# Optimization experiments

Hardware: AMD Instinct MI355X
Metric: run time of the kernel (lower is better)

Reference implementation:

```python
import jax, jax.numpy as jnp
import numpy as np
import math

HEADS = 4
LN_EPS = 1e-5


def _layer_norm(x, gamma, beta):
    # LayerNorm over last dim (N=4096), matching nn.LayerNorm(4096)
    mu = jnp.mean(x, axis=-1, keepdims=True)
    var = jnp.mean((x - mu) ** 2, axis=-1, keepdims=True)
    return (x - mu) * jax.lax.rsqrt(var + LN_EPS) * gamma + beta


def setup_inputs() -> dict:
    key = jax.random.key(0)
    ks = jax.random.split(key, 10)
    L, IMG, N = 1024, 1024, 4096
    s_img = 1.0 / math.sqrt(IMG)
    s_L = 1.0 / math.sqrt(L)
    return {
        "point_features": jax.random.normal(ks[0], (1, L, N), jnp.float32),
        "img_features": jax.random.normal(ks[1], (1, IMG, N), jnp.float32),
        # 4 per-head 1x1 convs IMG_chl -> L_chl
        "W_img": jax.random.normal(ks[2], (HEADS, L, IMG), jnp.float32) * s_img,
        "b_img": jax.random.normal(ks[3], (HEADS, L), jnp.float32) * s_img,
        # conv_L: L_chl -> L_chl
        "W_L": jax.random.normal(ks[4], (L, L), jnp.float32) * s_L,
        "b_L": jax.random.normal(ks[5], (L,), jnp.float32) * s_L,
        # LayerNorm(4096)
        "ln_g": jnp.ones((N,), jnp.float32),
        "ln_b": jnp.zeros((N,), jnp.float32),
        # conv_fusion: L_chl -> L_chl
        "W_f": jax.random.normal(ks[6], (L, L), jnp.float32) * s_L,
        "b_f": jax.random.normal(ks[7], (L,), jnp.float32) * s_L,
    }


def reference(point_features, img_features, W_img, b_img, W_L, b_L, ln_g, ln_b, W_f, b_f):
    # L_query = conv_L(point_features): [1, L, N]
    L_query = jnp.einsum('oi,bin->bon', W_L, point_features) + b_L[None, :, None]
    dk = L_query.shape[1]
    N = L_query.shape[2]

    # All 4 head keys at once: [H, 1, L, N]
    keys = jnp.einsum('hoi,bin->hbon', W_img, img_features) + b_img[:, None, :, None]

    # score_i = sum_c(key_i * query) / sqrt(dk)  -> cat over heads: [H, N] (B=1)
    score = jnp.sum(keys * L_query[None], axis=2).reshape(HEADS, N) / jnp.sqrt(jnp.float32(dk))

    # softmax across heads (dim=0), weightmap = [1, H, N]
    weight = jax.nn.softmax(score, axis=0)
    weightmap = weight[None]

    # z = sum_h weight[h] * key_h : [1, L, N]
    z = jnp.einsum('hn,hbcn->bcn', weight, keys)

    fused = _layer_norm(z + L_query, ln_g, ln_b)
    fusion_features = jnp.einsum('oi,bin->bon', W_f, fused) + b_f[None, :, None]
    return (fusion_features, weightmap)
```

## Files before the change

kernel.cpp:

```cpp
#include <hip/hip_runtime.h>
#include <hip/hip_bf16.h>
#include <stdint.h>

using u16 = unsigned short;

typedef __attribute__((ext_vector_type(8))) short bf16x8;
typedef __attribute__((ext_vector_type(4))) float f32x4;

typedef const __attribute__((address_space(1))) unsigned int* gas_t;
typedef __attribute__((address_space(3))) unsigned int* las_t;

__device__ inline void g2l16(const u16* g, u16* l) {
  __builtin_amdgcn_global_load_lds((gas_t)g, (las_t)l, 16, 0, 0);
}

__device__ inline u16 f2b(float x) {
  union { float f; uint32_t u; } v; v.f = x;
  uint32_t r = (v.u + 0x7FFFu + ((v.u >> 16) & 1u)) >> 16;
  return (u16)r;
}
__device__ inline float b2f(u16 b) {
  union { uint32_t u; float f; } v; v.u = ((uint32_t)b) << 16;
  return v.f;
}
__device__ inline float b2f_lo(uint32_t p) {
  union { uint32_t u; float f; } v; v.u = p << 16; return v.f;
}
__device__ inline float b2f_hi(uint32_t p) {
  union { uint32_t u; float f; } v; v.u = p & 0xFFFF0000u; return v.f;
}

__device__ inline void store_out(float* p, float v) { *p = v; }
__device__ inline void store_out(u16* p, float v) { *p = f2b(v); }

template<typename OutT>
__device__ inline void gemm_tile_128(const u16* __restrict__ A,
                                     const u16* __restrict__ Bt,
                                     const float* __restrict__ bias,
                                     OutT* __restrict__ C,
                                     int m0, int n0, int N, int K,
                                     u16* As, u16* Bs)
{
  const int tid  = threadIdx.x;
  const int wave = tid >> 6;
  const int lane = tid & 63;
  const int wm = wave >> 1, wn = wave & 1;
  const int lr = lane & 15;
  const int lq = lane >> 4;
  const int x7 = lr & 7;

  const int srow = tid >> 3;
  const int sgc  = (tid & 7) ^ (srow & 7);
  const u16* gA = A  + (size_t)(m0 + srow) * K + sgc * 8;
  const u16* gB = Bt + (size_t)(n0 + srow) * K + sgc * 8;
  u16* dstA = As + wave * 512;
  u16* dstB = Bs + wave * 512;

  f32x4 acc[4][4];
  #pragma unroll
  for (int i = 0; i < 4; ++i)
    #pragma unroll
    for (int j = 0; j < 4; ++j)
      acc[i][j] = (f32x4){0.f, 0.f, 0.f, 0.f};

  for (int k0 = 0; k0 < K; k0 += 64) {
    #pragma unroll
    for (int s = 0; s < 4; ++s) {
      g2l16(gA + (size_t)(s * 32) * K + k0, dstA + s * 2048);
      g2l16(gB + (size_t)(s * 32) * K + k0, dstB + s * 2048);
    }
    __syncthreads();

    #pragma unroll
    for (int ks = 0; ks < 2; ++ks) {
      const int pa = (ks * 4 + lq) ^ x7;
      bf16x8 af[4], bfr[4];
      #pragma unroll
      for (int im = 0; im < 4; ++im)
        af[im] = *(const bf16x8*)&As[(wm * 64 + im * 16 + lr) * 64 + pa * 8];
      #pragma unroll
      for (int in = 0; in < 4; ++in)
        bfr[in] = *(const bf16x8*)&Bs[(wn * 64 + in * 16 + lr) * 64 + pa * 8];

      #pragma unroll
      for (int im = 0; im < 4; ++im)
        #pragma unroll
        for (int in = 0; in < 4; ++in)
          acc[im][in] = __builtin_amdgcn_mfma_f32_16x16x32_bf16(
              af[im], bfr[in], acc[im][in], 0, 0, 0);
    }
    __syncthreads();
  }

  #pragma unroll
  for (int im = 0; im < 4; ++im) {
    const int mbase = m0 + wm * 64 + im * 16 + lq * 4;
    #pragma unroll
    for (int in = 0; in < 4; ++in) {
      const int ncol = n0 + wn * 64 + in * 16 + lr;
      #pragma unroll
      for (int r = 0; r < 4; ++r) {
        const int m = mbase + r;
        store_out(C + (size_t)m * N + ncol, acc[im][in][r] + bias[m]);
      }
    }
  }
}

__global__ __launch_bounds__(256)
void gemm_keys_q(const u16* __restrict__ WIb, const u16* __restrict__ IT,
                 const float* __restrict__ bim, u16* __restrict__ KEYS,
                 const u16* __restrict__ WLb, const u16* __restrict__ PT,
                 const float* __restrict__ bL, u16* __restrict__ Qb)
{
  __shared__ u16 As[128 * 64];
  __shared__ u16 Bs[128 * 64];
  const int by = blockIdx.y;
  const bool keys = (by < 32);
  const u16*   A    = keys ? WIb : WLb;
  const u16*   Bt   = keys ? IT  : PT;
  const float* bias = keys ? bim : bL;
  u16*         C    = keys ? KEYS : Qb;
  const int m0 = (by & 31) * 128;
  const int n0 = blockIdx.x * 128;
  gemm_tile_128<u16>(A, Bt, bias, C, m0, n0, 4096, 1024, As, Bs);
}

__global__ __launch_bounds__(256)
void gemm_f(const u16* __restrict__ A, const u16* __restrict__ Bt,
            const float* __restrict__ bias, float* __restrict__ C)
{
  __shared__ u16 As[128 * 64];
  __shared__ u16 Bs[128 * 64];
  gemm_tile_128<float>(A, Bt, bias, C, blockIdx.y * 128, blockIdx.x * 128,
                       4096, 1024, As, Bs);
}

__global__ __launch_bounds__(256)
void prep(const float* __restrict__ P, u16* __restrict__ PT,
          const float* __restrict__ I, u16* __restrict__ IT,
          const float4* __restrict__ wim, const float4* __restrict__ wl,
          const float4* __restrict__ wf, ushort4* __restrict__ wimb,
          ushort4* __restrict__ wlb, ushort4* __restrict__ wfb)
{
  const int bid = blockIdx.x;
  if (bid < 2048) {
    const int z   = bid >> 10;
    const int rem = bid & 1023;
    const int ct  = rem & 63;
    const int rt  = rem >> 6;
    const float* in = z ? I : P;
    u16* out = z ? IT : PT;
    __shared__ u16 tile[64][66];
    const int r0 = rt * 64, c0 = ct * 64;
    const int tr  = threadIdx.x >> 4;
    const int tc4 = threadIdx.x & 15;
    #pragma unroll
    for (int it = 0; it < 4; ++it) {
      const int r = it * 16 + tr;
      const float4 v = *(const float4*)&in[(size_t)(r0 + r) * 4096 + c0 + tc4 * 4];
      ushort4 o;
      o.x = f2b(v.x); o.y = f2b(v.y); o.z = f2b(v.z); o.w = f2b(v.w);
      *(ushort4*)&tile[r][tc4 * 4] = o;
    }
    __syncthreads();
    #pragma unroll
    for (int it = 0; it < 4; ++it) {
      const int c = it * 16 + tr;
      ushort4 o;
      o.x = tile[tc4 * 4 + 0][c];
      o.y = tile[tc4 * 4 + 1][c];
      o.z = tile[tc4 * 4 + 2][c];
      o.w = tile[tc4 * 4 + 3][c];
      *(ushort4*)&out[(size_t)(c0 + c) * 1024 + r0 + tc4 * 4] = o;
    }
  } else {
    int i = (bid - 2048) * 256 + threadIdx.x;
    const float4* src; ushort4* dst;
    if (i < 1048576)      { src = wim; dst = wimb; }
    else if (i < 1310720) { src = wl;  dst = wlb;  i -= 1048576; }
    else                  { src = wf;  dst = wfb;  i -= 1310720; }
    const float4 v = src[i];
    ushort4 o;
    o.x = f2b(v.x); o.y = f2b(v.y); o.z = f2b(v.z); o.w = f2b(v.w);
    dst[i] = o;
  }
}

__global__ __launch_bounds__(256)
void transpose_u16(const u16* __restrict__ in, u16* __restrict__ out,
                   int R, int C)
{
  __shared__ u16 tile[64][66];
  const int c0 = blockIdx.x * 64, r0 = blockIdx.y * 64;
  const int tr  = threadIdx.x >> 4;
  const int tc4 = threadIdx.x & 15;
  #pragma unroll
  for (int it = 0; it < 4; ++it) {
    const int r = it * 16 + tr;
    *(ushort4*)&tile[r][tc4 * 4] =
        *(const ushort4*)&in[(size_t)(r0 + r) * C + c0 + tc4 * 4];
  }
  __syncthreads();
  #pragma unroll
  for (int it = 0; it < 4; ++it) {
    const int c = it * 16 + tr;
    ushort4 o;
    o.x = tile[tc4 * 4 + 0][c];
    o.y = tile[tc4 * 4 + 1][c];
    o.z = tile[tc4 * 4 + 2][c];
    o.w = tile[tc4 * 4 + 3][c];
    *(ushort4*)&out[(size_t)(c0 + c) * R + r0 + tc4 * 4] = o;
  }
}

__global__ __launch_bounds__(256)
void score_partial(const u16* __restrict__ keys, const u16* __restrict__ Qb,
                   float* __restrict__ part)
{
  const int n  = blockIdx.x * 1024 + threadIdx.x * 4;
  const int c0 = blockIdx.y * 16;
  float s[4][4];
  #pragma unroll
  for (int h = 0; h < 4; ++h)
    #pragma unroll
    for (int e = 0; e < 4; ++e) s[h][e] = 0.f;

  for (int c = c0; c < c0 + 16; ++c) {
    const uint2 qv = *(const uint2*)&Qb[(size_t)c * 4096 + n];
    const float q0 = b2f_lo(qv.x), q1 = b2f_hi(qv.x);
    const float q2 = b2f_lo(qv.y), q3 = b2f_hi(qv.y);
    #pragma unroll
    for (int h = 0; h < 4; ++h) {
      const uint2 kv = *(const uint2*)&keys[((size_t)((h << 10) + c)) * 4096 + n];
      s[h][0] = fmaf(q0, b2f_lo(kv.x), s[h][0]);
      s[h][1] = fmaf(q1, b2f_hi(kv.x), s[h][1]);
      s[h][2] = fmaf(q2, b2f_lo(kv.y), s[h][2]);
      s[h][3] = fmaf(q3, b2f_hi(kv.y), s[h][3]);
    }
  }
  #pragma unroll
  for (int h = 0; h < 4; ++h) {
    float4 o;
    o.x = s[h][0] * 0.03125f; o.y = s[h][1] * 0.03125f;
    o.z = s[h][2] * 0.03125f; o.w = s[h][3] * 0.03125f;
    *(float4*)&part[((size_t)(blockIdx.y * 4 + h)) * 4096 + n] = o;
  }
}

__global__ __launch_bounds__(256)
void softmax_h(const float* __restrict__ part, float* __restrict__ wmap)
{
  __shared__ float red[4][4][64];
  const int nl = threadIdx.x & 63;
  const int cq = threadIdx.x >> 6;
  const int n  = blockIdx.x * 64 + nl;
  float s[4] = {0.f, 0.f, 0.f, 0.f};
  #pragma unroll
  for (int k = 0; k < 16; ++k) {
    const int cy = cq * 16 + k;
    const float* p = part + (size_t)cy * 16384 + n;
    s[0] += p[0]; s[1] += p[4096]; s[2] += p[8192]; s[3] += p[12288];
  }
  #pragma unroll
  for (int h = 0; h < 4; ++h) red[cq][h][nl] = s[h];
  __syncthreads();
  if (threadIdx.x < 64) {
    const float t0 = red[0][0][nl] + red[1][0][nl] + red[2][0][nl] + red[3][0][nl];
    const float t1 = red[0][1][nl] + red[1][1][nl] + red[2][1][nl] + red[3][1][nl];
    const float t2 = red[0][2][nl] + red[1][2][nl] + red[2][2][nl] + red[3][2][nl];
    const float t3 = red[0][3][nl] + red[1][3][nl] + red[2][3][nl] + red[3][3][nl];
    const float m = fmaxf(fmaxf(t0, t1), fmaxf(t2, t3));
    const float e0 = expf(t0 - m), e1 = expf(t1 - m);
    const float e2 = expf(t2 - m), e3 = expf(t3 - m);
    const float inv = 1.f / (e0 + e1 + e2 + e3);
    wmap[n] = e0 * inv; wmap[4096 + n] = e1 * inv;
    wmap[8192 + n] = e2 * inv; wmap[12288 + n] = e3 * inv;
  }
}

__global__ __launch_bounds__(256)
void z_ln(const u16* __restrict__ keys, const u16* __restrict__ Qb,
          const float* __restrict__ w, const float* __restrict__ g,
          const float* __restrict__ bb, u16* __restrict__ fused)
{
  const int c  = blockIdx.x;
  const int tx = threadIdx.x;
  float t[16];
  float s = 0.f, s2 = 0.f;
  #pragma unroll
  for (int j = 0; j < 2; ++j) {
    const int n = tx * 8 + j * 2048;
    const uint4 qv = *(const uint4*)&Qb[(size_t)c * 4096 + n];
    float z[8] = {0.f,0.f,0.f,0.f,0.f,0.f,0.f,0.f};
    #pragma unroll
    for (int h = 0; h < 4; ++h) {
      const uint4 kv = *(const uint4*)&keys[((size_t)((h << 10) + c)) * 4096 + n];
      const float4 w0 = *(const float4*)&w[h * 4096 + n];
      const float4 w1 = *(const float4*)&w[h * 4096 + n + 4];
      z[0] = fmaf(w0.x, b2f_lo(kv.x), z[0]);
      z[1] = fmaf(w0.y, b2f_hi(kv.x), z[1]);
      z[2] = fmaf(w0.z, b2f_lo(kv.y), z[2]);
      z[3] = fmaf(w0.w, b2f_hi(kv.y), z[3]);
      z[4] = fmaf(w1.x, b2f_lo(kv.z), z[4]);
      z[5] = fmaf(w1.y, b2f_hi(kv.z), z[5]);
      z[6] = fmaf(w1.z, b2f_lo(kv.w), z[6]);
      z[7] = fmaf(w1.w, b2f_hi(kv.w), z[7]);
    }
    const uint32_t qs[4] = {qv.x, qv.y, qv.z, qv.w};
    #pragma unroll
    for (int e = 0; e < 4; ++e) {
      const float v0 = z[2 * e]     + b2f_lo(qs[e]);
      const float v1 = z[2 * e + 1] + b2f_hi(qs[e]);
      t[8 * j + 2 * e]     = v0;
      t[8 * j + 2 * e + 1] = v1;
      s += v0 + v1;
      s2 = fmaf(v0, v0, fmaf(v1, v1, s2));
    }
  }
  #pragma unroll
  for (int o = 32; o > 0; o >>= 1) {
    s  += __shfl_down(s, o);
    s2 += __shfl_down(s2, o);
  }
  __shared__ float rbuf[8];
  const int wave = tx >> 6, lane = tx & 63;
  if (lane == 0) { rbuf[wave] = s; rbuf[4 + wave] = s2; }
  __syncthreads();
  s  = rbuf[0] + rbuf[1] + rbuf[2] + rbuf[3];
  s2 = rbuf[4] + rbuf[5] + rbuf[6] + rbuf[7];
  const float mu  = s * (1.f / 4096.f);
  const float var = s2 * (1.f / 4096.f) - mu * mu;
  const float rs  = rsqrtf(var + 1e-5f);
  #pragma unroll
  for (int j = 0; j < 2; ++j) {
    const int n = tx * 8 + j * 2048;
    #pragma unroll
    for (int q4 = 0; q4 < 2; ++q4) {
      const float4 gv = *(const float4*)&g[n + 4 * q4];
      const float4 bv = *(const float4*)&bb[n + 4 * q4];
      ushort4 o;
      o.x = f2b((t[8 * j + 4 * q4]     - mu) * rs * gv.x + bv.x);
      o.y = f2b((t[8 * j + 4 * q4 + 1] - mu) * rs * gv.y + bv.y);
      o.z = f2b((t[8 * j + 4 * q4 + 2] - mu) * rs * gv.z + bv.z);
      o.w = f2b((t[8 * j + 4 * q4 + 3] - mu) * rs * gv.w + bv.w);
      *(ushort4*)&fused[(size_t)c * 4096 + n + 4 * q4] = o;
    }
  }
}

extern "C" void kernel_launch(void* const* d_in, const int* in_sizes, int n_in,
                              void* d_out, int out_size, void* d_ws, size_t ws_size,
                              hipStream_t stream)
{
  const float* P   = (const float*)d_in[0];
  const float* I   = (const float*)d_in[1];
  const float* Wim = (const float*)d_in[2];
  const float* bim = (const float*)d_in[3];
  const float* WL  = (const float*)d_in[4];
  const float* bL  = (const float*)d_in[5];
  const float* lng = (const float*)d_in[6];
  const float* lnb = (const float*)d_in[7];
  const float* Wf  = (const float*)d_in[8];
  const float* bf_ = (const float*)d_in[9];
  float* out = (float*)d_out;

  char* ws = (char*)d_ws;
  u16*   PT     = (u16*)(ws + 0);
  u16*   IT     = (u16*)(ws + (size_t)8  * 1048576);
  u16*   WLb    = (u16*)(ws + (size_t)16 * 1048576);
  u16*   WIb    = (u16*)(ws + (size_t)18 * 1048576);
  u16*   WFb    = (u16*)(ws + (size_t)26 * 1048576);
  u16*   Qb     = (u16*)(ws + (size_t)28 * 1048576);
  u16*   KEYS   = (u16*)(ws + (size_t)36 * 1048576);
  float* PART   = (float*)(ws + 0);
  u16*   FUSED  = (u16*)(ws + (size_t)70 * 1048576);
  u16*   FUSEDT = (u16*)(ws + (size_t)78 * 1048576);

  const dim3 b256(256);

  prep<<<8192, b256, 0, stream>>>(P, PT, I, IT,
                                  (const float4*)Wim, (const float4*)WL,
                                  (const float4*)Wf, (ushort4*)WIb,
                                  (ushort4*)WLb, (ushort4*)WFb);

  gemm_keys_q<<<dim3(32, 40), b256, 0, stream>>>(WIb, IT, bim, KEYS,
                                                 WLb, PT, bL, Qb);

  score_partial<<<dim3(4, 64), b256, 0, stream>>>(KEYS, Qb, PART);
  float* wmap = out + (size_t)1024 * 4096;
  softmax_h<<<64, b256, 0, stream>>>(PART, wmap);

  z_ln<<<1024, b256, 0, stream>>>(KEYS, Qb, wmap, lng, lnb, FUSED);
  transpose_u16<<<dim3(64, 16), b256, 0, stream>>>(FUSED, FUSEDT, 1024, 4096);

  gemm_f<<<dim3(32, 8), b256, 0, stream>>>(WFb, FUSEDT, bf_, out);
}
```

Measured before the change: 227.9 us.

## Triple-buffer GEMM LDS tiles with async prefetch two K-steps ahead

Replaces the single-buffered K=64 GEMM loop with a three-slot ring of K=32 LDS tiles. Global-to-LDS loads are issued two iterations ahead, and a partial vmcnt wait plus one barrier per step replaces the two syncthreads. The LDS swizzle is reworked for 32-wide rows. The aim is to hide global load latency behind MFMA work, at the cost of more loop iterations and more LDS use per block.

After: 251.8 us. +10.5%, slower.

```diff
diff --git a/kernel.cpp b/kernel.cpp
--- a/kernel.cpp
+++ b/kernel.cpp
@@ -32,6 +32,8 @@
 
 __device__ inline void store_out(float* p, float v) { *p = v; }
 __device__ inline void store_out(u16* p, float v) { *p = f2b(v); }
+
+#define CFENCE asm volatile("" ::: "memory")
 
 template<typename OutT>
 __device__ inline void gemm_tile_128(const u16* __restrict__ A,
@@ -47,14 +49,13 @@
   const int wm = wave >> 1, wn = wave & 1;
   const int lr = lane & 15;
   const int lq = lane >> 4;
-  const int x7 = lr & 7;
-
-  const int srow = tid >> 3;
-  const int sgc  = (tid & 7) ^ (srow & 7);
+  const int pa8 = ((lq ^ ((lr ^ (lr >> 2)) & 3))) * 8;
+
+  const int srow = tid >> 2;
+  const int sgc  = (tid & 3) ^ ((srow ^ (srow >> 2)) & 3);
   const u16* gA = A  + (size_t)(m0 + srow) * K + sgc * 8;
   const u16* gB = Bt + (size_t)(n0 + srow) * K + sgc * 8;
-  u16* dstA = As + wave * 512;
-  u16* dstB = Bs + wave * 512;
+  const int ldst = wave * 512;
 
   f32x4 acc[4][4];
   #pragma unroll
@@ -63,33 +64,58 @@
     for (int j = 0; j < 4; ++j)
       acc[i][j] = (f32x4){0.f, 0.f, 0.f, 0.f};
 
-  for (int k0 = 0; k0 < K; k0 += 64) {
-    #pragma unroll
-    for (int s = 0; s < 4; ++s) {
-      g2l16(gA + (size_t)(s * 32) * K + k0, dstA + s * 2048);
-      g2l16(gB + (size_t)(s * 32) * K + k0, dstB + s * 2048);
-    }
-    __syncthreads();
-
-    #pragma unroll
-    for (int ks = 0; ks < 2; ++ks) {
-      const int pa = (ks * 4 + lq) ^ x7;
-      bf16x8 af[4], bfr[4];
-      #pragma unroll
-      for (int im = 0; im < 4; ++im)
-        af[im] = *(const bf16x8*)&As[(wm * 64 + im * 16 + lr) * 64 + pa * 8];
+  auto STAGE = [&](int slot, int kt) {
+    const size_t ko = (size_t)kt * 32;
+    u16* da = As + slot * 4096 + ldst;
+    u16* db = Bs + slot * 4096 + ldst;
+    g2l16(gA + ko,                  da);
+    g2l16(gA + (size_t)64 * K + ko, da + 2048);
+    g2l16(gB + ko,                  db);
+    g2l16(gB + (size_t)64 * K + ko, db + 2048);
+  };
+
+  const int NT = K >> 5;
+
+  STAGE(0, 0);
+  STAGE(1, 1);
+  asm volatile("s_waitcnt vmcnt(4)" ::: "memory");
+  CFENCE;
+  __builtin_amdgcn_s_barrier();
+  CFENCE;
+
+  int sc = 0;
+  int sn = 2;
+  for (int t = 0; t < NT; ++t) {
+    const bool more = (t + 2 < NT);
+    if (more) STAGE(sn, t + 2);
+
+    const u16* ab = As + sc * 4096;
+    const u16* bb = Bs + sc * 4096;
+    bf16x8 af[4], bfr[4];
+    #pragma unroll
+    for (int im = 0; im < 4; ++im)
+      af[im] = *(const bf16x8*)&ab[(wm * 64 + im * 16 + lr) * 32 + pa8];
+    #pragma unroll
+    for (int in = 0; in < 4; ++in)
+      bfr[in] = *(const bf16x8*)&bb[(wn * 64 + in * 16 + lr) * 32 + pa8];
+
+    #pragma unroll
+    for (int im = 0; im < 4; ++im)
       #pragma unroll
       for (int in = 0; in < 4; ++in)
-        bfr[in] = *(const bf16x8*)&Bs[(wn * 64 + in * 16 + lr) * 64 + pa * 8];
-
-      #pragma unroll
-      for (int im = 0; im < 4; ++im)
-        #pragma unroll
-        for (int in = 0; in < 4; ++in)
-          acc[im][in] = __builtin_amdgcn_mfma_f32_16x16x32_bf16(
-              af[im], bfr[in], acc[im][in], 0, 0, 0);
-    }
-    __syncthreads();
+        acc[im][in] = __builtin_amdgcn_mfma_f32_16x16x32_bf16(
+            af[im], bfr[in], acc[im][in], 0, 0, 0);
+
+    if (more)
+      asm volatile("s_waitcnt vmcnt(4)" ::: "memory");
+    else
+      asm volatile("s_waitcnt vmcnt(0)" ::: "memory");
+    CFENCE;
+    __builtin_amdgcn_s_barrier();
+    CFENCE;
+
+    sc = (sc + 1 == 3) ? 0 : sc + 1;
+    sn = (sn + 1 == 3) ? 0 : sn + 1;
   }
 
   #pragma unroll
@@ -113,8 +139,8 @@
                  const u16* __restrict__ WLb, const u16* __restrict__ PT,
                  const float* __restrict__ bL, u16* __restrict__ Qb)
 {
-  __shared__ u16 As[128 * 64];
-  __shared__ u16 Bs[128 * 64];
+  __shared__ u16 As[3 * 128 * 32];
+  __shared__ u16 Bs[3 * 128 * 32];
   const int by = blockIdx.y;
   const bool keys = (by < 32);
   const u16*   A    = keys ? WIb : WLb;
@@ -130,8 +156,8 @@
 void gemm_f(const u16* __restrict__ A, const u16* __restrict__ Bt,
             const float* __restrict__ bias, float* __restrict__ C)
 {
-  __shared__ u16 As[128 * 64];
-  __shared__ u16 Bs[128 * 64];
+  __shared__ u16 As[3 * 128 * 32];
+  __shared__ u16 Bs[3 * 128 * 32];
   gemm_tile_128<float>(A, Bt, bias, C, blockIdx.y * 128, blockIdx.x * 128,
                        4096, 1024, As, Bs);
 }
```
